# Kernel tuning notes

Measured on AMD Instinct MI355X. Metric: run time of the kernel, lower is better.

## Reference

```python
import jax, jax.numpy as jnp
import numpy as np

# Regular (3,6) rate-1/2 LDPC Tanner graph
N = 8192        # variable nodes (codeword length n)
R = 4096        # check nodes (r = n - k)
DV = 3          # variable-node degree
DC = 6          # check-node degree
E = N * DV      # number of edges (= R * DC)
B = 1024        # batch of codewords decoded simultaneously
ITERS = 10      # fixed BP iterations (max_iterations; early-exit dropped for jit)
CLIP = 0.999    # original clips the tanh-product to (-0.999, 0.999)


def setup_inputs() -> dict:
    rng = np.random.default_rng(0)
    # Edge list of a regular bipartite graph: each var appears DV times,
    # each check appears DC times; random socket permutation (Gallager style).
    edge_var = np.repeat(np.arange(N, dtype=np.int32), DV)
    edge_check = rng.permutation(np.repeat(np.arange(R, dtype=np.int32), DC))
    key = jax.random.key(0)
    received = jax.random.normal(key, (B, N), dtype=jnp.float32)
    return {
        "received": received,
        "edge_var": jnp.asarray(edge_var),
        "edge_check": jnp.asarray(edge_check),
    }


def reference(received, edge_var, edge_check):
    """Batched sum-product (belief propagation) LDPC decoding.

    received: [B, N] soft channel values; noise_variance = 1.0.
    Messages live on edges, shape [E, B].
    """
    noise_variance = 1.0
    llr = 2.0 * received / noise_variance            # [B, N] channel LLRs
    llr_t = llr.T                                     # [N, B]

    v2c0 = llr_t[edge_var]                            # [E, B] initial var->check msgs
    c2v0 = jnp.zeros_like(v2c0)                       # [E, B] initial check->var msgs

    def body(i, carry):
        v2c, _ = carry
        # --- check-node update: leave-one-out product of tanh(msg/2) ---
        t = jnp.tanh(0.5 * v2c)                       # [E, B]
        prod_c = jax.ops.segment_prod(t, edge_check, num_segments=R)  # [R, B]
        loo = prod_c[edge_check] / t                  # leave-one-out product, [E, B]
        c2v = 2.0 * jnp.arctanh(jnp.clip(loo, -CLIP, CLIP))
        # --- variable-node update: leave-one-out sum of check msgs + channel ---
        tot = llr_t + jax.ops.segment_sum(c2v, edge_var, num_segments=N)  # [N, B]
        v2c_new = tot[edge_var] - c2v                 # [E, B]
        return (v2c_new, c2v)

    _, c2v = jax.lax.fori_loop(0, ITERS, body, (v2c0, c2v0))

    # Final posterior LLRs: channel LLR + sum of incoming check->var msgs
    final_llrs = llr + jax.ops.segment_sum(c2v, edge_var, num_segments=N).T  # [B, N]
    decoded_bits = (final_llrs < 0).astype(jnp.int32)
    return final_llrs, decoded_bits
```

## Files before the change

### kernel.cpp

```cpp
#include <hip/hip_runtime.h>


#define N_  8192
#define R_  4096
#define DV_ 3
#define DC_ 6
#define E_  (N_ * DV_)
#define B_  1024
#define ITERS_ 10

#define THREADS_ 1024
#define CPT_ (R_ / THREADS_)
#define VPT_ (N_ / THREADS_)

#define LOG2E_ 1.442695041f
#define LN2_   0.69314718f

__device__ __forceinline__ unsigned lds_off(const void* p) {
  return (unsigned)(unsigned long long)p;
}

__global__ __launch_bounds__(256) void build_edges_kernel(
    const int* __restrict__ edge_check, unsigned int* __restrict__ counters,
    int* __restrict__ check_edges) {
  int e = blockIdx.x * 256 + threadIdx.x;
  if (e < E_) {
    int r = edge_check[e];
    unsigned int ret = atomicAdd(&counters[r], 1u);
    check_edges[r * DC_ + (ret % 6u)] = e;
  }
}

__device__ __forceinline__ void issue_reads6(float dst[DC_],
                                             const unsigned ra[DC_]) {
  asm volatile("ds_read_b32 %0, %1" : "=v"(dst[0]) : "v"(ra[0]));
  asm volatile("ds_read_b32 %0, %1" : "=v"(dst[1]) : "v"(ra[1]));
  asm volatile("ds_read_b32 %0, %1" : "=v"(dst[2]) : "v"(ra[2]));
  asm volatile("ds_read_b32 %0, %1" : "=v"(dst[3]) : "v"(ra[3]));
  asm volatile("ds_read_b32 %0, %1" : "=v"(dst[4]) : "v"(ra[4]));
  asm volatile("ds_read_b32 %0, %1" : "=v"(dst[5]) : "v"(ra[5]));
}

__device__ __forceinline__ void compute_check(const float Ev[DC_],
                                              float qo[DC_],
                                              const unsigned wa[DC_]) {
  float t[DC_];
#pragma unroll
  for (int i = 0; i < DC_; i++)
    t[i] = (Ev[i] - qo[i]) * __builtin_amdgcn_rcpf(Ev[i] + qo[i]);
  float loo[DC_];
  float run = 1.0f;
#pragma unroll
  for (int i = 0; i < DC_; i++) { loo[i] = run; run *= t[i]; }
  run = 1.0f;
#pragma unroll
  for (int i = DC_ - 1; i >= 0; i--) { loo[i] *= run; run *= t[i]; }
#pragma unroll
  for (int i = 0; i < DC_; i++) {
    float y = __builtin_amdgcn_fmed3f(loo[i], -0.999f, 0.999f);
    float qq = (1.0f + y) * __builtin_amdgcn_rcpf(1.0f - y);
    asm volatile("ds_write_b32 %0, %1" :: "v"(wa[i]), "v"(qq));
    qo[i] = qq;
  }
}

__global__ __launch_bounds__(THREADS_, 4) void persistent_kernel(
    const float* __restrict__ recv, const int* __restrict__ check_edges,
    float* __restrict__ out) {
  __shared__ float E_s[N_];
  __shared__ float q_s[E_];
  const int b = blockIdx.x;
  const int tid = threadIdx.x;
  const float* r = recv + (size_t)b * N_;

  int eidx[CPT_][DC_];
#pragma unroll
  for (int c = 0; c < CPT_; c++) {
    int rr = c * THREADS_ + tid;
    int e0 = check_edges[rr * DC_ + 0], e1 = check_edges[rr * DC_ + 1];
    int e2 = check_edges[rr * DC_ + 2], e3 = check_edges[rr * DC_ + 3];
    int e4 = check_edges[rr * DC_ + 4], e5 = check_edges[rr * DC_ + 5];
#define CSWAP(a, b) { int lo = min(a, b), hi = max(a, b); a = lo; b = hi; }
    CSWAP(e0, e5) CSWAP(e1, e3) CSWAP(e2, e4)
    CSWAP(e1, e2) CSWAP(e3, e4)
    CSWAP(e0, e3) CSWAP(e2, e5)
    CSWAP(e0, e1) CSWAP(e2, e3) CSWAP(e4, e5)
    CSWAP(e1, e2) CSWAP(e3, e4)
#undef CSWAP
    eidx[c][0] = e0; eidx[c][1] = e1; eidx[c][2] = e2;
    eidx[c][3] = e3; eidx[c][4] = e4; eidx[c][5] = e5;
  }

  unsigned raddr[CPT_][DC_], waddr[CPT_][DC_];
#pragma unroll
  for (int c = 0; c < CPT_; c++)
#pragma unroll
    for (int i = 0; i < DC_; i++) {
      raddr[c][i] = lds_off(&E_s[(unsigned)eidx[c][i] / 3u]);
      waddr[c][i] = lds_off(&q_s[eidx[c][i]]);
      asm volatile("" : "+v"(raddr[c][i]), "+v"(waddr[c][i]));
    }

  float qown[CPT_][DC_];
#pragma unroll
  for (int c = 0; c < CPT_; c++)
#pragma unroll
    for (int i = 0; i < DC_; i++) qown[c][i] = 1.0f;

  float e_llr[VPT_];
#pragma unroll
  for (int k = 0; k < VPT_; k++) {
    float llr = 2.0f * r[tid + k * THREADS_];
    e_llr[k] = __builtin_amdgcn_exp2f(llr * LOG2E_);
    E_s[tid + k * THREADS_] = e_llr[k];
  }
  __syncthreads();

  for (int iter = 0; iter < ITERS_; iter++) {
    float Ev0[DC_], Ev1[DC_], Ev2[DC_], Ev3[DC_];
    issue_reads6(Ev0, raddr[0]);

    issue_reads6(Ev1, raddr[1]);
    asm volatile("s_waitcnt lgkmcnt(6)" ::: "memory");
    __builtin_amdgcn_sched_barrier(0);
    compute_check(Ev0, qown[0], waddr[0]);

    issue_reads6(Ev2, raddr[2]);
    asm volatile("s_waitcnt lgkmcnt(12)" ::: "memory");
    __builtin_amdgcn_sched_barrier(0);
    compute_check(Ev1, qown[1], waddr[1]);

    issue_reads6(Ev3, raddr[3]);
    asm volatile("s_waitcnt lgkmcnt(12)" ::: "memory");
    __builtin_amdgcn_sched_barrier(0);
    compute_check(Ev2, qown[2], waddr[2]);

    asm volatile("s_waitcnt lgkmcnt(6)" ::: "memory");
    __builtin_amdgcn_sched_barrier(0);
    compute_check(Ev3, qown[3], waddr[3]);

    asm volatile("s_waitcnt lgkmcnt(0)" ::: "memory");
    __syncthreads();

#pragma unroll
    for (int k = 0; k < VPT_; k++) {
      int v = tid + k * THREADS_;
      float2 q01;
      __builtin_memcpy(&q01, &q_s[3 * v], sizeof(float2));
      float q2 = q_s[3 * v + 2];
      E_s[v] = ((e_llr[k] * q01.x) * q01.y) * q2;
    }
    __syncthreads();
  }

  const size_t BN = (size_t)B_ * N_;
#pragma unroll
  for (int k = 0; k < VPT_; k++) {
    int n = tid + k * THREADS_;
    float val = LN2_ * __builtin_amdgcn_logf(E_s[n]);
    out[(size_t)b * N_ + n] = val;
    out[BN + (size_t)b * N_ + n] = (val < 0.0f) ? 1.0f : 0.0f;
  }
}

extern "C" void kernel_launch(void* const* d_in, const int* in_sizes, int n_in,
                              void* d_out, int out_size, void* d_ws,
                              size_t ws_size, hipStream_t stream) {
  const float* recv = (const float*)d_in[0];
  const int* edge_check = (const int*)d_in[2];
  float* out = (float*)d_out;

  char* ws = (char*)d_ws;
  unsigned int* counters = (unsigned int*)ws;
  int* check_edges = (int*)(ws + (size_t)R_ * sizeof(unsigned int));

  build_edges_kernel<<<(E_ + 255) / 256, 256, 0, stream>>>(edge_check, counters,
                                                           check_edges);
  persistent_kernel<<<B_, THREADS_, 0, stream>>>(recv, check_edges, out);
}
```

Before: 231.5 us.

## Reorder check-edge slots to balance LDS bank conflicts across each wavefront

Adds a single-block preprocessing kernel that, for each wavefront's 64 checks, greedily assigns each check's six edges to slot positions so that, per slot, the E_s read banks and q_s write banks are spread evenly across the 32 banks. The persistent decoder then reads the edge order as-is, without its own sort. The aim is fewer LDS bank conflicts in the inner check-node reads and writes. The cost is an extra serial kernel launch with 64 threads each looping over 64 checks, which adds fixed latency to every call.

Result: slower. 374.2 us (+61.6%).

```diff
diff --git a/kernel.cpp b/kernel.cpp
--- a/kernel.cpp
+++ b/kernel.cpp
@@ -31,52 +31,17 @@
   }
 }
 
-__device__ __forceinline__ void issue_reads6(float dst[DC_],
-                                             const unsigned ra[DC_]) {
-  asm volatile("ds_read_b32 %0, %1" : "=v"(dst[0]) : "v"(ra[0]));
-  asm volatile("ds_read_b32 %0, %1" : "=v"(dst[1]) : "v"(ra[1]));
-  asm volatile("ds_read_b32 %0, %1" : "=v"(dst[2]) : "v"(ra[2]));
-  asm volatile("ds_read_b32 %0, %1" : "=v"(dst[3]) : "v"(ra[3]));
-  asm volatile("ds_read_b32 %0, %1" : "=v"(dst[4]) : "v"(ra[4]));
-  asm volatile("ds_read_b32 %0, %1" : "=v"(dst[5]) : "v"(ra[5]));
-}
-
-__device__ __forceinline__ void compute_check(const float Ev[DC_],
-                                              float qo[DC_],
-                                              const unsigned wa[DC_]) {
-  float t[DC_];
+__global__ __launch_bounds__(64) void schedule_kernel(
+    int* __restrict__ check_edges) {
+  __shared__ unsigned char loads[64][DC_][64];
+  const int u = threadIdx.x;
 #pragma unroll
   for (int i = 0; i < DC_; i++)
-    t[i] = (Ev[i] - qo[i]) * __builtin_amdgcn_rcpf(Ev[i] + qo[i]);
-  float loo[DC_];
-  float run = 1.0f;
-#pragma unroll
-  for (int i = 0; i < DC_; i++) { loo[i] = run; run *= t[i]; }
-  run = 1.0f;
-#pragma unroll
-  for (int i = DC_ - 1; i >= 0; i--) { loo[i] *= run; run *= t[i]; }
-#pragma unroll
-  for (int i = 0; i < DC_; i++) {
-    float y = __builtin_amdgcn_fmed3f(loo[i], -0.999f, 0.999f);
-    float qq = (1.0f + y) * __builtin_amdgcn_rcpf(1.0f - y);
-    asm volatile("ds_write_b32 %0, %1" :: "v"(wa[i]), "v"(qq));
-    qo[i] = qq;
-  }
-}
-
-__global__ __launch_bounds__(THREADS_, 4) void persistent_kernel(
-    const float* __restrict__ recv, const int* __restrict__ check_edges,
-    float* __restrict__ out) {
-  __shared__ float E_s[N_];
-  __shared__ float q_s[E_];
-  const int b = blockIdx.x;
-  const int tid = threadIdx.x;
-  const float* r = recv + (size_t)b * N_;
-
-  int eidx[CPT_][DC_];
-#pragma unroll
-  for (int c = 0; c < CPT_; c++) {
-    int rr = c * THREADS_ + tid;
+    for (int b = 0; b < 64; b++) loads[u][i][b] = 0;
+  const int c = u & 3;
+  const int w = u >> 2;
+  for (int l = 0; l < 64; l++) {
+    const int rr = c * 1024 + (w << 6) + l;
     int e0 = check_edges[rr * DC_ + 0], e1 = check_edges[rr * DC_ + 1];
     int e2 = check_edges[rr * DC_ + 2], e3 = check_edges[rr * DC_ + 3];
     int e4 = check_edges[rr * DC_ + 4], e5 = check_edges[rr * DC_ + 5];
@@ -87,8 +52,77 @@
     CSWAP(e0, e1) CSWAP(e2, e3) CSWAP(e4, e5)
     CSWAP(e1, e2) CSWAP(e3, e4)
 #undef CSWAP
-    eidx[c][0] = e0; eidx[c][1] = e1; eidx[c][2] = e2;
-    eidx[c][3] = e3; eidx[c][4] = e4; eidx[c][5] = e5;
+    unsigned used = 0;
+#define ASSIGN(ej)                                                         \
+    {                                                                      \
+      unsigned br = ((unsigned)(ej) / 3u) & 31u;                           \
+      unsigned bw = (unsigned)(ej) & 31u;                                  \
+      int best = 0, bestcost = 1 << 30;                                    \
+      _Pragma("unroll")                                                    \
+      for (int i = 0; i < DC_; i++) {                                      \
+        if (!((used >> i) & 1u)) {                                         \
+          int cost = (int)loads[u][i][br] + (int)loads[u][i][32 + bw];     \
+          if (cost < bestcost) { bestcost = cost; best = i; }              \
+        }                                                                  \
+      }                                                                    \
+      used |= 1u << best;                                                  \
+      loads[u][best][br]++;                                                \
+      loads[u][best][32 + bw]++;                                           \
+      check_edges[rr * DC_ + best] = (ej);                                 \
+    }
+    ASSIGN(e0) ASSIGN(e1) ASSIGN(e2) ASSIGN(e3) ASSIGN(e4) ASSIGN(e5)
+#undef ASSIGN
+  }
+}
+
+__device__ __forceinline__ void issue_reads6(float dst[DC_],
+                                             const unsigned ra[DC_]) {
+  asm volatile("ds_read_b32 %0, %1" : "=v"(dst[0]) : "v"(ra[0]));
+  asm volatile("ds_read_b32 %0, %1" : "=v"(dst[1]) : "v"(ra[1]));
+  asm volatile("ds_read_b32 %0, %1" : "=v"(dst[2]) : "v"(ra[2]));
+  asm volatile("ds_read_b32 %0, %1" : "=v"(dst[3]) : "v"(ra[3]));
+  asm volatile("ds_read_b32 %0, %1" : "=v"(dst[4]) : "v"(ra[4]));
+  asm volatile("ds_read_b32 %0, %1" : "=v"(dst[5]) : "v"(ra[5]));
+}
+
+__device__ __forceinline__ void compute_check(const float Ev[DC_],
+                                              float qo[DC_],
+                                              const unsigned wa[DC_]) {
+  float t[DC_];
+#pragma unroll
+  for (int i = 0; i < DC_; i++)
+    t[i] = (Ev[i] - qo[i]) * __builtin_amdgcn_rcpf(Ev[i] + qo[i]);
+  float loo[DC_];
+  float run = 1.0f;
+#pragma unroll
+  for (int i = 0; i < DC_; i++) { loo[i] = run; run *= t[i]; }
+  run = 1.0f;
+#pragma unroll
+  for (int i = DC_ - 1; i >= 0; i--) { loo[i] *= run; run *= t[i]; }
+#pragma unroll
+  for (int i = 0; i < DC_; i++) {
+    float y = __builtin_amdgcn_fmed3f(loo[i], -0.999f, 0.999f);
+    float qq = (1.0f + y) * __builtin_amdgcn_rcpf(1.0f - y);
+    asm volatile("ds_write_b32 %0, %1" :: "v"(wa[i]), "v"(qq));
+    qo[i] = qq;
+  }
+}
+
+__global__ __launch_bounds__(THREADS_, 4) void persistent_kernel(
+    const float* __restrict__ recv, const int* __restrict__ check_edges,
+    float* __restrict__ out) {
+  __shared__ float E_s[N_];
+  __shared__ float q_s[E_];
+  const int b = blockIdx.x;
+  const int tid = threadIdx.x;
+  const float* r = recv + (size_t)b * N_;
+
+  int eidx[CPT_][DC_];
+#pragma unroll
+  for (int c = 0; c < CPT_; c++) {
+    int rr = c * THREADS_ + tid;
+#pragma unroll
+    for (int i = 0; i < DC_; i++) eidx[c][i] = check_edges[rr * DC_ + i];
   }
 
   unsigned raddr[CPT_][DC_], waddr[CPT_][DC_];
@@ -98,7 +132,6 @@
     for (int i = 0; i < DC_; i++) {
       raddr[c][i] = lds_off(&E_s[(unsigned)eidx[c][i] / 3u]);
       waddr[c][i] = lds_off(&q_s[eidx[c][i]]);
-      asm volatile("" : "+v"(raddr[c][i]), "+v"(waddr[c][i]));
     }
 
   float qown[CPT_][DC_];
@@ -176,5 +209,6 @@
 
   build_edges_kernel<<<(E_ + 255) / 256, 256, 0, stream>>>(edge_check, counters,
                                                            check_edges);
+  schedule_kernel<<<1, 64, 0, stream>>>(check_edges);
   persistent_kernel<<<B_, THREADS_, 0, stream>>>(recv, check_edges, out);
 }
```
